# Kernel optimization log

Measured on AMD Instinct MI355X. Metric: run time of the kernel, lower is better.

## Reference

```python
import jax, jax.numpy as jnp
import numpy as np

N_NODES = 50000
N_EDGES = 800000
IN_DIM, HID, HEADS = 3, 64, 4
NEG_SLOPE = 0.2  # PyG GATConv default leaky_relu slope


def _glorot(key, shape):
    fan_in, fan_out = shape[0], shape[-1]
    lim = (6.0 / (fan_in + fan_out)) ** 0.5
    return jax.random.uniform(key, shape, jnp.float32, -lim, lim)


def setup_inputs() -> dict:
    key = jax.random.key(0)
    ks = jax.random.split(key, 12)
    x = jax.random.normal(ks[0], (N_NODES, IN_DIM), jnp.float32)
    edge_index = jax.random.randint(ks[1], (2, N_EDGES), 0, N_NODES, jnp.int64)
    return {
        "x": x,
        "edge_index": edge_index,
        "W1": _glorot(ks[2], (IN_DIM, HEADS * HID)),
        "a_src1": _glorot(ks[3], (HEADS, HID)),
        "a_dst1": _glorot(ks[4], (HEADS, HID)),
        "b1": jnp.zeros((HEADS * HID,), jnp.float32),
        "W2": _glorot(ks[5], (HEADS * HID, HID)),
        "a_src2": _glorot(ks[6], (1, HID)),
        "a_dst2": _glorot(ks[7], (1, HID)),
        "b2": jnp.zeros((HID,), jnp.float32),
        # fc: 64 -> 1
        "Wfc": _glorot(ks[8], (HID, 1)),
        "bfc": jnp.zeros((1,), jnp.float32),
    }


def _gat_layer(x, src, dst, W, a_src, a_dst, b, heads, out_ch, n):
    # h: [N, H, C]
    h = (x @ W).reshape(n, heads, out_ch)
    # per-node attention halves, gathered per edge -> [E, H]
    alpha_s = jnp.einsum("nhc,hc->nh", h, a_src)
    alpha_d = jnp.einsum("nhc,hc->nh", h, a_dst)
    e = jax.nn.leaky_relu(alpha_s[src] + alpha_d[dst], NEG_SLOPE)
    # numerically stable segment softmax over incoming edges of each dst node
    e_max = jax.ops.segment_max(e, dst, num_segments=n)
    ex = jnp.exp(e - e_max[dst])
    denom = jax.ops.segment_sum(ex, dst, num_segments=n)
    alpha = ex / (denom[dst] + 1e-16)  # [E, H]
    # weighted scatter-aggregate of source features
    msg = h[src] * alpha[:, :, None]  # [E, H, C]
    out = jax.ops.segment_sum(msg, dst, num_segments=n)  # [N, H, C]
    return out.reshape(n, heads * out_ch) + b


def reference(x, edge_index, W1, a_src1, a_dst1, b1, W2, a_src2, a_dst2, b2, Wfc, bfc):
    n = x.shape[0]
    # PyG GATConv adds self-loops by default
    loops = jnp.arange(n, dtype=edge_index.dtype)
    src = jnp.concatenate([edge_index[0], loops])
    dst = jnp.concatenate([edge_index[1], loops])
    # dropout layers are identity in eval mode
    h = _gat_layer(x, src, dst, W1, a_src1, a_dst1, b1, HEADS, HID, n)
    h = jax.nn.elu(h)
    h = _gat_layer(h, src, dst, W2, a_src2, a_dst2, b2, 1, HID, n)
    h = jax.nn.elu(h)
    out = jax.nn.sigmoid(h @ Wfc + bfc)
    return out.squeeze(-1)
```

## Files before the change

kernel.cpp:

```cpp
#include <hip/hip_runtime.h>
#include <hip/hip_fp16.h>
#include <math.h>

#define N_NODES 50000
#define N_EDGES 800000
#define E_TOT   (N_EDGES + N_NODES)
#define NEG_SLOPE 0.2f

#define CNT_OFF    0UL
#define ZERO_BYTES 200000UL
#define CSR_OFF    200000UL
#define VS1_OFF    6600000UL
#define VD1_OFF    6600064UL
#define AS1_OFF    6600160UL
#define AD1_OFF    7400160UL
#define X2_OFF     8200160UL
#define H2_OFF     33800160UL
#define AS2_OFF    40200160UL
#define AD2_OFF    40400160UL

__device__ __forceinline__ float wave_reduce_sum(float v) {
    #pragma unroll
    for (int off = 32; off > 0; off >>= 1) v += __shfl_xor(v, off, 64);
    return v;
}
__device__ __forceinline__ float grp_reduce_sum(float v) {
    #pragma unroll
    for (int off = 8; off > 0; off >>= 1) v += __shfl_xor(v, off, 64);
    return v;
}
__device__ __forceinline__ float lrelu(float v) { return v > 0.f ? v : NEG_SLOPE * v; }
__device__ __forceinline__ float elu(float v)   { return v > 0.f ? v : __expf(v) - 1.f; }

__global__ void precompute_folds(const float* __restrict__ W1, const float* __restrict__ a_s1,
                                 const float* __restrict__ a_d1,
                                 float* __restrict__ vs1, float* __restrict__ vd1) {
    int t = threadIdx.x, h = t >> 6, lane = t & 63;
    float avs = a_s1[h*64 + lane], avd = a_d1[h*64 + lane];
    #pragma unroll
    for (int k = 0; k < 3; ++k) {
        float w = W1[k*256 + h*64 + lane];
        float ps = wave_reduce_sum(w * avs);
        float pd = wave_reduce_sum(w * avd);
        if (lane == 0) { vs1[k*4+h] = ps; vd1[k*4+h] = pd; }
    }
}

__global__ void node_alpha1(const float* __restrict__ x, const float* __restrict__ vs,
                            const float* __restrict__ vd, float* __restrict__ as1,
                            float* __restrict__ ad1) {
    int n = blockIdx.x*blockDim.x + threadIdx.x;
    if (n >= N_NODES) return;
    float x0 = x[n*3+0], x1 = x[n*3+1], x2v = x[n*3+2];
    float4 s, d;
    s.x = x0*vs[0] + x1*vs[4] + x2v*vs[8];
    s.y = x0*vs[1] + x1*vs[5] + x2v*vs[9];
    s.z = x0*vs[2] + x1*vs[6] + x2v*vs[10];
    s.w = x0*vs[3] + x1*vs[7] + x2v*vs[11];
    d.x = x0*vd[0] + x1*vd[4] + x2v*vd[8];
    d.y = x0*vd[1] + x1*vd[5] + x2v*vd[9];
    d.z = x0*vd[2] + x1*vd[6] + x2v*vd[10];
    d.w = x0*vd[3] + x1*vd[7] + x2v*vd[11];
    *(float4*)(as1 + (size_t)n*4) = s;
    *(float4*)(ad1 + (size_t)n*4) = d;
}

__global__ void build_csr(const int* __restrict__ ei, unsigned* __restrict__ cnt,
                          unsigned short* __restrict__ csr) {
    int tid = blockIdx.x*blockDim.x + threadIdx.x;
    int base = tid * 8;
    if (base >= E_TOT) return;
    if (base < N_EDGES) {
        int4 sa = *(const int4*)(ei + base);
        int4 sb = *(const int4*)(ei + base + 4);
        int4 da = *(const int4*)(ei + N_EDGES + base);
        int4 db = *(const int4*)(ei + N_EDGES + base + 4);
        int ss[8] = {sa.x,sa.y,sa.z,sa.w,sb.x,sb.y,sb.z,sb.w};
        int dd[8] = {da.x,da.y,da.z,da.w,db.x,db.y,db.z,db.w};
        #pragma unroll
        for (int i = 0; i < 8; ++i) {
            unsigned p = atomicAdd(&cnt[dd[i]], 1u);
            if (p < 64u) csr[((size_t)dd[i] << 6) + p] = (unsigned short)ss[i];
        }
    } else {
        #pragma unroll
        for (int i = 0; i < 8; ++i) {
            int v = base + i - N_EDGES;
            unsigned p = atomicAdd(&cnt[v], 1u);
            if (p < 64u) csr[((size_t)v << 6) + p] = (unsigned short)v;
        }
    }
}

__global__ void gat1_node(const unsigned short* __restrict__ csr, const unsigned* __restrict__ cnt,
                          const float* __restrict__ x, const float* __restrict__ W1,
                          const float* __restrict__ as1, const float* __restrict__ ad1,
                          const float* __restrict__ b1, __half* __restrict__ x2out) {
    int lane = threadIdx.x & 63, w = threadIdx.x >> 6;
    int subl = lane & 15, grp = lane >> 4;
    int n = blockIdx.x*16 + w*4 + grp;
    unsigned deg = min(cnt[n], 64u);
    const unsigned short* row = csr + ((size_t)n << 6);
    float4 adv = *(const float4*)(ad1 + (size_t)n*4);
    float d0=0.f, d1=0.f, d2=0.f, d3=0.f;
    float g00=0,g01=0,g02=0, g10=0,g11=0,g12=0, g20=0,g21=0,g22=0, g30=0,g31=0,g32=0;
    for (unsigned c = subl; c < deg; c += 16) {
        int s = row[c];
        float4 as = *(const float4*)(as1 + (size_t)s*4);
        float e0 = __expf(lrelu(as.x+adv.x));
        float e1 = __expf(lrelu(as.y+adv.y));
        float e2 = __expf(lrelu(as.z+adv.z));
        float e3 = __expf(lrelu(as.w+adv.w));
        float xa = x[s*3+0], xb = x[s*3+1], xc = x[s*3+2];
        d0 += e0; d1 += e1; d2 += e2; d3 += e3;
        g00 = fmaf(e0,xa,g00); g01 = fmaf(e0,xb,g01); g02 = fmaf(e0,xc,g02);
        g10 = fmaf(e1,xa,g10); g11 = fmaf(e1,xb,g11); g12 = fmaf(e1,xc,g12);
        g20 = fmaf(e2,xa,g20); g21 = fmaf(e2,xb,g21); g22 = fmaf(e2,xc,g22);
        g30 = fmaf(e3,xa,g30); g31 = fmaf(e3,xb,g31); g32 = fmaf(e3,xc,g32);
    }
    float r_0 = 1.f/(grp_reduce_sum(d0) + 1e-16f);
    float r_1 = 1.f/(grp_reduce_sum(d1) + 1e-16f);
    float r_2 = 1.f/(grp_reduce_sum(d2) + 1e-16f);
    float r_3 = 1.f/(grp_reduce_sum(d3) + 1e-16f);
    g00 = grp_reduce_sum(g00)*r_0; g01 = grp_reduce_sum(g01)*r_0; g02 = grp_reduce_sum(g02)*r_0;
    g10 = grp_reduce_sum(g10)*r_1; g11 = grp_reduce_sum(g11)*r_1; g12 = grp_reduce_sum(g12)*r_1;
    g20 = grp_reduce_sum(g20)*r_2; g21 = grp_reduce_sum(g21)*r_2; g22 = grp_reduce_sum(g22)*r_2;
    g30 = grp_reduce_sum(g30)*r_3; g31 = grp_reduce_sum(g31)*r_3; g32 = grp_reduce_sum(g32)*r_3;
    __half* xrow = x2out + (size_t)n*256;
    #pragma unroll
    for (int i = 0; i < 16; ++i) {
        int j = i*16 + subl;
        float ga, gb, gc;
        if      (i < 4)  { ga=g00; gb=g01; gc=g02; }
        else if (i < 8)  { ga=g10; gb=g11; gc=g12; }
        else if (i < 12) { ga=g20; gb=g21; gc=g22; }
        else             { ga=g30; gb=g31; gc=g32; }
        float val = ga*W1[j] + gb*W1[256+j] + gc*W1[512+j] + b1[j];
        xrow[j] = __float2half(elu(val));
    }
}

#define KB 32
__global__ __launch_bounds__(256) void node_prep2(
        const __half* __restrict__ x2, const float* __restrict__ W2,
        __half* __restrict__ h2) {
    __shared__ float xT[KB][68];
    __shared__ float Wt[KB][64];
    int t = threadIdx.x;
    int n0 = blockIdx.x * 64;
    int i = t & 15, j = t >> 4;
    float acc[4][4] = {{0,0,0,0},{0,0,0,0},{0,0,0,0},{0,0,0,0}};
    for (int k0 = 0; k0 < 256; k0 += KB) {
        __syncthreads();
        {
            int node = t >> 2, g8 = t & 3;
            int nr = n0 + node; if (nr >= N_NODES) nr = N_NODES - 1;
            float4 raw = *(const float4*)(x2 + (size_t)nr*256 + k0 + g8*8);
            const __half2* hp = (const __half2*)&raw;
            #pragma unroll
            for (int q = 0; q < 4; ++q) {
                float2 f = __half22float2(hp[q]);
                xT[g8*8 + 2*q + 0][node] = f.x;
                xT[g8*8 + 2*q + 1][node] = f.y;
            }
        }
        int p = t;
        #pragma unroll
        for (int rr = 0; rr < 2; ++rr, p += 256) {
            int kr = p >> 4, c4 = p & 15;
            *(float4*)(&Wt[kr][c4*4]) = *(const float4*)(W2 + (size_t)(k0+kr)*64 + c4*4);
        }
        __syncthreads();
        #pragma unroll
        for (int k = 0; k < KB; ++k) {
            float4 xv = *(const float4*)(&xT[k][4*i]);
            float4 wv = *(const float4*)(&Wt[k][4*j]);
            acc[0][0]=fmaf(xv.x,wv.x,acc[0][0]); acc[0][1]=fmaf(xv.x,wv.y,acc[0][1]);
            acc[0][2]=fmaf(xv.x,wv.z,acc[0][2]); acc[0][3]=fmaf(xv.x,wv.w,acc[0][3]);
            acc[1][0]=fmaf(xv.y,wv.x,acc[1][0]); acc[1][1]=fmaf(xv.y,wv.y,acc[1][1]);
            acc[1][2]=fmaf(xv.y,wv.z,acc[1][2]); acc[1][3]=fmaf(xv.y,wv.w,acc[1][3]);
            acc[2][0]=fmaf(xv.z,wv.x,acc[2][0]); acc[2][1]=fmaf(xv.z,wv.y,acc[2][1]);
            acc[2][2]=fmaf(xv.z,wv.z,acc[2][2]); acc[2][3]=fmaf(xv.z,wv.w,acc[2][3]);
            acc[3][0]=fmaf(xv.w,wv.x,acc[3][0]); acc[3][1]=fmaf(xv.w,wv.y,acc[3][1]);
            acc[3][2]=fmaf(xv.w,wv.z,acc[3][2]); acc[3][3]=fmaf(xv.w,wv.w,acc[3][3]);
        }
    }
    #pragma unroll
    for (int ii = 0; ii < 4; ++ii) {
        int n = n0 + 4*i + ii;
        if (n < N_NODES) {
            union { __half2 h[2]; float2 f; } u;
            u.h[0] = __floats2half2_rn(acc[ii][0], acc[ii][1]);
            u.h[1] = __floats2half2_rn(acc[ii][2], acc[ii][3]);
            *(float2*)(h2 + (size_t)n*64 + 4*j) = u.f;
        }
    }
}

__global__ void node_alpha2(const __half* __restrict__ h2, const float* __restrict__ a_s2,
                            const float* __restrict__ a_d2, float* __restrict__ as2,
                            float* __restrict__ ad2) {
    int lane = threadIdx.x & 63, w = threadIdx.x >> 6;
    int n = blockIdx.x*4 + w;
    float v = __half2float(h2[(size_t)n*64 + lane]);
    float ps = wave_reduce_sum(v * a_s2[lane]);
    float pd = wave_reduce_sum(v * a_d2[lane]);
    if (lane == 0) { as2[n] = ps; ad2[n] = pd; }
}

__global__ void gat2_node(const unsigned short* __restrict__ csr, const unsigned* __restrict__ cnt,
                          const __half* __restrict__ h2, const float* __restrict__ as2,
                          const float* __restrict__ ad2, const float* __restrict__ b2,
                          const float* __restrict__ Wfc, const float* __restrict__ bfc,
                          float* __restrict__ out) {
    int lane = threadIdx.x & 63, w = threadIdx.x >> 6;
    int n = blockIdx.x*4 + w;
    unsigned deg = min(cnt[n], 64u);
    const unsigned short* row = csr + ((size_t)n << 6);
    float adv = ad2[n];
    int s_l = 0; float ex_l = 0.f;
    if (lane < (int)deg) {
        s_l = row[lane];
        ex_l = __expf(lrelu(as2[s_l] + adv));
    }
    float den = wave_reduce_sum(ex_l);
    float acc = 0.f;
    unsigned degr = (deg + 7u) & ~7u;
    for (unsigned c = 0; c < degr; c += 8) {
        #pragma unroll
        for (int u = 0; u < 8; ++u) {
            int e = (int)c + u;
            float ex = __shfl(ex_l, e, 64);
            int   s  = __shfl(s_l,  e, 64);
            float hv = __half2float(h2[((size_t)s << 6) + lane]);
            acc = fmaf(hv, ex, acc);
        }
    }
    float v = elu(acc/(den + 1e-16f) + b2[lane]);
    float part = wave_reduce_sum(v * Wfc[lane]);
    if (lane == 0) out[n] = 1.f/(1.f + __expf(-(part + bfc[0])));
}

extern "C" void kernel_launch(void* const* d_in, const int* in_sizes, int n_in,
                              void* d_out, int out_size, void* d_ws, size_t ws_size,
                              hipStream_t stream) {
    const float* x      = (const float*)d_in[0];
    const int*   ei     = (const int*)  d_in[1];
    const float* W1     = (const float*)d_in[2];
    const float* a_src1 = (const float*)d_in[3];
    const float* a_dst1 = (const float*)d_in[4];
    const float* b1     = (const float*)d_in[5];
    const float* W2     = (const float*)d_in[6];
    const float* a_src2 = (const float*)d_in[7];
    const float* a_dst2 = (const float*)d_in[8];
    const float* b2     = (const float*)d_in[9];
    const float* Wfc    = (const float*)d_in[10];
    const float* bfc    = (const float*)d_in[11];
    float* out = (float*)d_out;

    char* ws = (char*)d_ws;
    unsigned*       cnt  = (unsigned*)      (ws + CNT_OFF);
    unsigned short* csr  = (unsigned short*)(ws + CSR_OFF);
    float*          vs1  = (float*)         (ws + VS1_OFF);
    float*          vd1  = (float*)         (ws + VD1_OFF);
    float*          as1  = (float*)         (ws + AS1_OFF);
    float*          ad1  = (float*)         (ws + AD1_OFF);
    __half*         x2   = (__half*)        (ws + X2_OFF);
    __half*         h2   = (__half*)        (ws + H2_OFF);
    float*          as2  = (float*)         (ws + AS2_OFF);
    float*          ad2  = (float*)         (ws + AD2_OFF);

    hipMemsetAsync(d_ws, 0, ZERO_BYTES, stream);

    const int BLK = 256;
    precompute_folds<<<1, BLK, 0, stream>>>(W1, a_src1, a_dst1, vs1, vd1);
    node_alpha1 <<<(N_NODES + BLK - 1)/BLK, BLK, 0, stream>>>(x, vs1, vd1, as1, ad1);
    build_csr   <<<(E_TOT/8 + BLK - 1)/BLK, BLK, 0, stream>>>(ei, cnt, csr);
    gat1_node   <<<N_NODES/16, BLK, 0, stream>>>(csr, cnt, x, W1, as1, ad1, b1, x2);
    node_prep2  <<<(N_NODES + 63)/64, BLK, 0, stream>>>(x2, W2, h2);
    node_alpha2 <<<N_NODES/4, BLK, 0, stream>>>(h2, a_src2, a_dst2, as2, ad2);
    gat2_node   <<<N_NODES/4, BLK, 0, stream>>>(csr, cnt, h2, as2, ad2, b2, Wfc, bfc, out);
}
```

Before: 147.0 us.

## Slice CSR build by destination range and fold layer-2 attention into GEMM

The CSR build kernel now partitions destination nodes into 8 slices. Each block scans the whole edge list but only inserts edges whose destination falls in its slice, which aims to localise atomics and CSR writes in cache. Separately, W2 is pre-multiplied by a_src2 and a_dst2, so the layer-2 attention scalars are computed inside node_prep2 from the x2 tile already loaded, removing the node_alpha2 kernel. The slicing makes every slice read the destination array again (8 times over), and the folded attention now comes from fp16 x2 instead of h2, which changes rounding slightly.

New measurement: 138.1 us. 6.0% less time.

```diff
diff --git a/kernel.cpp b/kernel.cpp
--- a/kernel.cpp
+++ b/kernel.cpp
@@ -6,18 +6,23 @@
 #define N_EDGES 800000
 #define E_TOT   (N_EDGES + N_NODES)
 #define NEG_SLOPE 0.2f
+#define NSLICE 8
+#define NODES_PER_SLICE (N_NODES / NSLICE)
+#define SLICE_BLOCKS 256
 
 #define CNT_OFF    0UL
 #define ZERO_BYTES 200000UL
 #define CSR_OFF    200000UL
 #define VS1_OFF    6600000UL
 #define VD1_OFF    6600064UL
-#define AS1_OFF    6600160UL
-#define AD1_OFF    7400160UL
-#define X2_OFF     8200160UL
-#define H2_OFF     33800160UL
-#define AS2_OFF    40200160UL
-#define AD2_OFF    40400160UL
+#define VAS2_OFF   6600128UL
+#define VAD2_OFF   6601152UL
+#define AS1_OFF    6602176UL
+#define AD1_OFF    7402176UL
+#define X2_OFF     8202176UL
+#define H2_OFF     33802176UL
+#define AS2_OFF    40202176UL
+#define AD2_OFF    40402176UL
 
 __device__ __forceinline__ float wave_reduce_sum(float v) {
     #pragma unroll
@@ -33,8 +38,10 @@
 __device__ __forceinline__ float elu(float v)   { return v > 0.f ? v : __expf(v) - 1.f; }
 
 __global__ void precompute_folds(const float* __restrict__ W1, const float* __restrict__ a_s1,
-                                 const float* __restrict__ a_d1,
-                                 float* __restrict__ vs1, float* __restrict__ vd1) {
+                                 const float* __restrict__ a_d1, const float* __restrict__ W2,
+                                 const float* __restrict__ a_s2, const float* __restrict__ a_d2,
+                                 float* __restrict__ vs1, float* __restrict__ vd1,
+                                 float* __restrict__ vas2, float* __restrict__ vad2) {
     int t = threadIdx.x, h = t >> 6, lane = t & 63;
     float avs = a_s1[h*64 + lane], avd = a_d1[h*64 + lane];
     #pragma unroll
@@ -44,6 +51,13 @@
         float pd = wave_reduce_sum(w * avd);
         if (lane == 0) { vs1[k*4+h] = ps; vd1[k*4+h] = pd; }
     }
+    float ss = 0.f, dd = 0.f;
+    for (int c = 0; c < 64; ++c) {
+        float wv = W2[t*64 + c];
+        ss = fmaf(wv, a_s2[c], ss);
+        dd = fmaf(wv, a_d2[c], dd);
+    }
+    vas2[t] = ss; vad2[t] = dd;
 }
 
 __global__ void node_alpha1(const float* __restrict__ x, const float* __restrict__ vs,
@@ -67,28 +81,32 @@
 
 __global__ void build_csr(const int* __restrict__ ei, unsigned* __restrict__ cnt,
                           unsigned short* __restrict__ csr) {
-    int tid = blockIdx.x*blockDim.x + threadIdx.x;
-    int base = tid * 8;
-    if (base >= E_TOT) return;
-    if (base < N_EDGES) {
-        int4 sa = *(const int4*)(ei + base);
-        int4 sb = *(const int4*)(ei + base + 4);
-        int4 da = *(const int4*)(ei + N_EDGES + base);
-        int4 db = *(const int4*)(ei + N_EDGES + base + 4);
-        int ss[8] = {sa.x,sa.y,sa.z,sa.w,sb.x,sb.y,sb.z,sb.w};
-        int dd[8] = {da.x,da.y,da.z,da.w,db.x,db.y,db.z,db.w};
-        #pragma unroll
-        for (int i = 0; i < 8; ++i) {
-            unsigned p = atomicAdd(&cnt[dd[i]], 1u);
-            if (p < 64u) csr[((size_t)dd[i] << 6) + p] = (unsigned short)ss[i];
-        }
-    } else {
-        #pragma unroll
-        for (int i = 0; i < 8; ++i) {
-            int v = base + i - N_EDGES;
-            unsigned p = atomicAdd(&cnt[v], 1u);
-            if (p < 64u) csr[((size_t)v << 6) + p] = (unsigned short)v;
-        }
+    int slice = blockIdx.x & (NSLICE-1);
+    int bi    = blockIdx.x >> 3;
+    int lo = slice * NODES_PER_SLICE, hi = lo + NODES_PER_SLICE;
+    const int stride = SLICE_BLOCKS * 256;
+    for (int c = bi*256 + threadIdx.x; c < N_EDGES/4; c += stride) {
+        int4 d4 = *(const int4*)(ei + N_EDGES + c*4);
+        if (d4.x >= lo && d4.x < hi) {
+            unsigned p = atomicAdd(&cnt[d4.x], 1u);
+            if (p < 64u) csr[((size_t)d4.x << 6) + p] = (unsigned short)ei[c*4+0];
+        }
+        if (d4.y >= lo && d4.y < hi) {
+            unsigned p = atomicAdd(&cnt[d4.y], 1u);
+            if (p < 64u) csr[((size_t)d4.y << 6) + p] = (unsigned short)ei[c*4+1];
+        }
+        if (d4.z >= lo && d4.z < hi) {
+            unsigned p = atomicAdd(&cnt[d4.z], 1u);
+            if (p < 64u) csr[((size_t)d4.z << 6) + p] = (unsigned short)ei[c*4+2];
+        }
+        if (d4.w >= lo && d4.w < hi) {
+            unsigned p = atomicAdd(&cnt[d4.w], 1u);
+            if (p < 64u) csr[((size_t)d4.w << 6) + p] = (unsigned short)ei[c*4+3];
+        }
+    }
+    for (int v = lo + bi*256 + threadIdx.x; v < hi; v += stride) {
+        unsigned p = atomicAdd(&cnt[v], 1u);
+        if (p < 64u) csr[((size_t)v << 6) + p] = (unsigned short)v;
     }
 }
 
@@ -143,25 +161,32 @@
 #define KB 32
 __global__ __launch_bounds__(256) void node_prep2(
         const __half* __restrict__ x2, const float* __restrict__ W2,
-        __half* __restrict__ h2) {
+        const float* __restrict__ vas2, const float* __restrict__ vad2,
+        __half* __restrict__ h2, float* __restrict__ as2, float* __restrict__ ad2) {
     __shared__ float xT[KB][68];
     __shared__ float Wt[KB][64];
     int t = threadIdx.x;
     int n0 = blockIdx.x * 64;
     int i = t & 15, j = t >> 4;
+    int snode = t >> 2, g8 = t & 3;
+    int snr = n0 + snode; if (snr >= N_NODES) snr = N_NODES - 1;
     float acc[4][4] = {{0,0,0,0},{0,0,0,0},{0,0,0,0},{0,0,0,0}};
+    float pas = 0.f, pad = 0.f;
     for (int k0 = 0; k0 < 256; k0 += KB) {
         __syncthreads();
         {
-            int node = t >> 2, g8 = t & 3;
-            int nr = n0 + node; if (nr >= N_NODES) nr = N_NODES - 1;
-            float4 raw = *(const float4*)(x2 + (size_t)nr*256 + k0 + g8*8);
+            float4 raw = *(const float4*)(x2 + (size_t)snr*256 + k0 + g8*8);
             const __half2* hp = (const __half2*)&raw;
             #pragma unroll
             for (int q = 0; q < 4; ++q) {
                 float2 f = __half22float2(hp[q]);
-                xT[g8*8 + 2*q + 0][node] = f.x;
-                xT[g8*8 + 2*q + 1][node] = f.y;
+                int kk = g8*8 + 2*q;
+                xT[kk+0][snode] = f.x;
+                xT[kk+1][snode] = f.y;
+                pas = fmaf(f.x, vas2[k0+kk],   pas);
+                pas = fmaf(f.y, vas2[k0+kk+1], pas);
+                pad = fmaf(f.x, vad2[k0+kk],   pad);
+                pad = fmaf(f.y, vad2[k0+kk+1], pad);
             }
         }
         int p = t;
@@ -185,6 +210,9 @@
             acc[3][2]=fmaf(xv.w,wv.z,acc[3][2]); acc[3][3]=fmaf(xv.w,wv.w,acc[3][3]);
         }
     }
+    pas += __shfl_xor(pas, 1, 64); pas += __shfl_xor(pas, 2, 64);
+    pad += __shfl_xor(pad, 1, 64); pad += __shfl_xor(pad, 2, 64);
+    if (g8 == 0 && n0 + snode < N_NODES) { as2[n0+snode] = pas; ad2[n0+snode] = pad; }
     #pragma unroll
     for (int ii = 0; ii < 4; ++ii) {
         int n = n0 + 4*i + ii;
@@ -195,17 +223,6 @@
             *(float2*)(h2 + (size_t)n*64 + 4*j) = u.f;
         }
     }
-}
-
-__global__ void node_alpha2(const __half* __restrict__ h2, const float* __restrict__ a_s2,
-                            const float* __restrict__ a_d2, float* __restrict__ as2,
-                            float* __restrict__ ad2) {
-    int lane = threadIdx.x & 63, w = threadIdx.x >> 6;
-    int n = blockIdx.x*4 + w;
-    float v = __half2float(h2[(size_t)n*64 + lane]);
-    float ps = wave_reduce_sum(v * a_s2[lane]);
-    float pd = wave_reduce_sum(v * a_d2[lane]);
-    if (lane == 0) { as2[n] = ps; ad2[n] = pd; }
 }
 
 __global__ void gat2_node(const unsigned short* __restrict__ csr, const unsigned* __restrict__ cnt,
@@ -263,6 +280,8 @@
     unsigned short* csr  = (unsigned short*)(ws + CSR_OFF);
     float*          vs1  = (float*)         (ws + VS1_OFF);
     float*          vd1  = (float*)         (ws + VD1_OFF);
+    float*          vas2 = (float*)         (ws + VAS2_OFF);
+    float*          vad2 = (float*)         (ws + VAD2_OFF);
     float*          as1  = (float*)         (ws + AS1_OFF);
     float*          ad1  = (float*)         (ws + AD1_OFF);
     __half*         x2   = (__half*)        (ws + X2_OFF);
@@ -273,11 +292,11 @@
     hipMemsetAsync(d_ws, 0, ZERO_BYTES, stream);
 
     const int BLK = 256;
-    precompute_folds<<<1, BLK, 0, stream>>>(W1, a_src1, a_dst1, vs1, vd1);
+    precompute_folds<<<1, BLK, 0, stream>>>(W1, a_src1, a_dst1, W2, a_src2, a_dst2,
+                                            vs1, vd1, vas2, vad2);
     node_alpha1 <<<(N_NODES + BLK - 1)/BLK, BLK, 0, stream>>>(x, vs1, vd1, as1, ad1);
-    build_csr   <<<(E_TOT/8 + BLK - 1)/BLK, BLK, 0, stream>>>(ei, cnt, csr);
+    build_csr   <<<NSLICE*SLICE_BLOCKS, BLK, 0, stream>>>(ei, cnt, csr);
     gat1_node   <<<N_NODES/16, BLK, 0, stream>>>(csr, cnt, x, W1, as1, ad1, b1, x2);
-    node_prep2  <<<(N_NODES + 63)/64, BLK, 0, stream>>>(x2, W2, h2);
-    node_alpha2 <<<N_NODES/4, BLK, 0, stream>>>(h2, a_src2, a_dst2, as2, ad2);
+    node_prep2  <<<(N_NODES + 63)/64, BLK, 0, stream>>>(x2, W2, vas2, vad2, h2, as2, ad2);
     gat2_node   <<<N_NODES/4, BLK, 0, stream>>>(csr, cnt, h2, as2, ad2, b2, Wfc, bfc, out);
 }
```
